# Kernel tuning notes

Measured on AMD Instinct MI355X. Metric: run time of the kernel, lower is better.

## Reference

```python
import jax, jax.numpy as jnp
import numpy as np

N_NODES = 100000
N_EDGES = 1600000


def setup_inputs() -> dict:
    key = jax.random.key(0)
    ks = jax.random.split(key, 6)
    x = jax.random.normal(ks[0], (N_NODES, 128), dtype=jnp.float32)
    edge_src = jax.random.randint(ks[1], (N_EDGES,), 0, N_NODES, dtype=jnp.int64)
    edge_dst = jax.random.randint(ks[2], (N_EDGES,), 0, N_NODES, dtype=jnp.int64)
    # GCNConv weights (bias=False); glorot-like scaling
    W1 = jax.random.normal(ks[3], (128, 64), dtype=jnp.float32) * (1.0 / np.sqrt(128))
    W2 = jax.random.normal(ks[4], (64, 64), dtype=jnp.float32) * (1.0 / np.sqrt(64))
    W3 = jax.random.normal(ks[5], (64, 40), dtype=jnp.float32) * (1.0 / np.sqrt(64))
    return {"x": x, "edge_src": edge_src, "edge_dst": edge_dst,
            "W1": W1, "W2": W2, "W3": W3}


def reference(x, edge_src, edge_dst, W1, W2, W3):
    # SGC forward (eval mode: dropout is identity).
    # Each GCNConv(normalize=False, bias=False): out = A @ (h @ W)
    n = x.shape[0]

    def conv(h, W):
        hw = h @ W                      # [N, d_out] dense transform
        msgs = hw[edge_src]             # [E, d_out] gather over edges
        return jax.ops.segment_sum(msgs, edge_dst, num_segments=n)  # scatter-add

    h = conv(x, W1)
    h = conv(h, W2)
    h = conv(h, W3)
    return jax.nn.log_softmax(h, axis=-1)
```

## Files before the change

kernel.cpp:

```cpp
#include <hip/hip_runtime.h>
#include <hip/hip_fp16.h>
#include <math.h>


#define BW    128
#define NBMAX 1024
#define BCAP  3072
#define D     40
#define RS    64

typedef unsigned short u16;
typedef unsigned int   u32;

__global__ void k_w12(const float* __restrict__ W1, const float* __restrict__ W2,
                      float* __restrict__ W12, int* __restrict__ gcnt) {
    int idx = blockIdx.x * blockDim.x + threadIdx.x;
    if (blockIdx.x == 0) {
        for (int i = threadIdx.x; i < NBMAX; i += blockDim.x) gcnt[i] = 0;
    }
    if (idx >= 128 * 64) return;
    int r = idx >> 6, c = idx & 63;
    float acc = 0.f;
#pragma unroll
    for (int k = 0; k < 64; ++k) acc += W1[r * 64 + k] * W2[k * 64 + c];
    W12[idx] = acc;
}

__global__ void k_wc(const float* __restrict__ W12, const float* __restrict__ W3,
                     float* __restrict__ Wc) {
    int idx = blockIdx.x * blockDim.x + threadIdx.x;
    if (idx >= 128 * 40) return;
    int r = idx / 40, c = idx - r * 40;
    float acc = 0.f;
#pragma unroll
    for (int k = 0; k < 64; ++k) acc += W12[r * 64 + k] * W3[k * 40 + c];
    Wc[idx] = acc;
}

__global__ void k_gemm(const float4* __restrict__ x4, const float4* __restrict__ Wc4,
                       u16* __restrict__ yout, int n_nodes) {
    __shared__ float4 wc[128 * 10];
    for (int i = threadIdx.x; i < 1280; i += blockDim.x) wc[i] = Wc4[i];
    __syncthreads();
    int tid = blockIdx.x * blockDim.x + threadIdx.x;
    int node = tid / 5, j0 = tid - node * 5;
    if (node >= n_nodes) return;
    float4 a0 = {0.f, 0.f, 0.f, 0.f}, a1 = {0.f, 0.f, 0.f, 0.f};
    const float4* xr = x4 + (size_t)node * 32;
#pragma unroll
    for (int k4 = 0; k4 < 32; ++k4) {
        float4 v = xr[k4];
#pragma unroll
        for (int kk = 0; kk < 4; ++kk) {
            float c = (kk == 0) ? v.x : (kk == 1) ? v.y : (kk == 2) ? v.z : v.w;
            float4 w0 = wc[(k4 * 4 + kk) * 10 + j0 * 2];
            float4 w1 = wc[(k4 * 4 + kk) * 10 + j0 * 2 + 1];
            a0.x += c * w0.x; a0.y += c * w0.y; a0.z += c * w0.z; a0.w += c * w0.w;
            a1.x += c * w1.x; a1.y += c * w1.y; a1.z += c * w1.z; a1.w += c * w1.w;
        }
    }
    __half2 h0 = __floats2half2_rn(a0.x, a0.y);
    __half2 h1 = __floats2half2_rn(a0.z, a0.w);
    __half2 h2 = __floats2half2_rn(a1.x, a1.y);
    __half2 h3 = __floats2half2_rn(a1.z, a1.w);
    uint4 st;
    st.x = *(u32*)&h0; st.y = *(u32*)&h1; st.z = *(u32*)&h2; st.w = *(u32*)&h3;
    *(uint4*)(yout + (size_t)node * RS + j0 * 8) = st;
}

#define PCHUNK 2048
__global__ void k_part(const int* __restrict__ src, const int* __restrict__ dst,
                       int* __restrict__ gcnt, int* __restrict__ part,
                       int E, int nb) {
    __shared__ int h[NBMAX];
    __shared__ int base[NBMAX];
    int t = threadIdx.x;
    int e0 = blockIdx.x * PCHUNK;
    int e1 = min(e0 + PCHUNK, E);
    for (int i = t; i < nb; i += 256) h[i] = 0;
    __syncthreads();
    for (int e = e0 + t; e < e1; e += 256)
        atomicAdd(&h[dst[e] >> 7], 1);
    __syncthreads();
    for (int i = t; i < nb; i += 256) {
        int c = h[i];
        base[i] = c ? atomicAdd(&gcnt[i], c) : 0;
    }
    __syncthreads();
    for (int i = t; i < nb; i += 256) h[i] = 0;
    __syncthreads();
    for (int e = e0 + t; e < e1; e += 256) {
        int d = dst[e];
        int b = d >> 7;
        int p = base[b] + atomicAdd(&h[b], 1);
        if (p < BCAP) part[(size_t)b * BCAP + p] = (src[e] << 7) | (d & 127);
    }
}

__global__ void k_csr(const int* __restrict__ part, const int* __restrict__ gcnt,
                      int* __restrict__ begv, int* __restrict__ endv,
                      int* __restrict__ ssort, int N) {
    __shared__ int cnt[BW];
    __shared__ int pos[BW];
    __shared__ int cur[BW];
    __shared__ int wsum[2];
    int b = blockIdx.x, t = threadIdx.x;
    int m = min(gcnt[b], BCAP);
    const int* bp = part + (size_t)b * BCAP;
    if (t < BW) cnt[t] = 0;
    __syncthreads();
    for (int k = t; k < m; k += 256)
        atomicAdd(&cnt[bp[k] & 127], 1);
    __syncthreads();
    int v = 0, inc = 0;
    if (t < BW) {
        v = cnt[t];
        inc = v;
#pragma unroll
        for (int off = 1; off < 64; off <<= 1) {
            int u = __shfl_up(inc, off, 64);
            if ((t & 63) >= off) inc += u;
        }
        if ((t & 63) == 63) wsum[t >> 6] = inc;
    }
    __syncthreads();
    int node0 = b * BW;
    if (t < BW) {
        int local = ((t >= 64) ? wsum[0] : 0) + inc - v;
        pos[t] = local;
        cur[t] = 0;
        if (node0 + t < N) {
            begv[node0 + t] = b * BCAP + local;
            endv[node0 + t] = b * BCAP + local + v;
        }
    }
    __syncthreads();
    for (int k = t; k < m; k += 256) {
        int p = bp[k];
        int r = p & 127;
        int loc = atomicAdd(&cur[r], 1);
        ssort[(size_t)b * BCAP + pos[r] + loc] = p >> 7;
    }
}

template <int FINAL>
__global__ void k_agg(const u16* __restrict__ yin, void* __restrict__ youtv,
                      const int* __restrict__ begv, const int* __restrict__ endv,
                      const int* __restrict__ srcs, int n_nodes) {
    int wid = (blockIdx.x * blockDim.x + threadIdx.x) >> 6;
    int lane = threadIdx.x & 63;
    if (wid >= n_nodes) return;
    int beg = begv[wid];
    int deg = endv[wid] - beg;
    int g = lane / 10;
    int sub = lane - g * 10;
    bool act = (g < 6);
    const char* base = (const char*)yin + sub * 8;
    int sv = (lane < deg) ? srcs[beg + lane] : 0;
    __half2 c0 = __floats2half2_rn(0.f, 0.f);
    __half2 c1 = __floats2half2_rn(0.f, 0.f);
    int dlim = min(deg, 64);
    for (int k = 0; k < dlim; k += 24) {
#pragma unroll
        for (int j = 0; j < 4; ++j) {
            int e = k + g + 6 * j;
            int es = (e < dlim) ? e : 0;
            int s = __shfl(sv, es, 64);
            if (act && e < dlim) {
                uint2 w = *(const uint2*)(base + (size_t)((u32)s * 128u));
                c0 = __hadd2(c0, *(__half2*)&w.x);
                c1 = __hadd2(c1, *(__half2*)&w.y);
            }
        }
    }
    for (int k = 64 + g; k < deg; k += 6) {
        if (act) {
            uint2 w = *(const uint2*)(base + (size_t)((u32)srcs[beg + k] * 128u));
            c0 = __hadd2(c0, *(__half2*)&w.x);
            c1 = __hadd2(c1, *(__half2*)&w.y);
        }
    }
    float2 f0 = __half22float2(c0);
    float2 f1 = __half22float2(c1);
    float a0 = f0.x, a1 = f0.y, a2 = f1.x, a3 = f1.y;
    float b0 = a0 + __shfl(a0, lane + 30, 64);
    float b1 = a1 + __shfl(a1, lane + 30, 64);
    float b2 = a2 + __shfl(a2, lane + 30, 64);
    float b3 = a3 + __shfl(a3, lane + 30, 64);
    float s0 = b0 + __shfl(b0, lane + 10, 64) + __shfl(b0, lane + 20, 64);
    float s1 = b1 + __shfl(b1, lane + 10, 64) + __shfl(b1, lane + 20, 64);
    float s2 = b2 + __shfl(b2, lane + 10, 64) + __shfl(b2, lane + 20, 64);
    float s3 = b3 + __shfl(b3, lane + 10, 64) + __shfl(b3, lane + 20, 64);
    if (FINAL) {
        float m = fmaxf(fmaxf(s0, s1), fmaxf(s2, s3));
        float mv = (lane < 10) ? m : -INFINITY;
#pragma unroll
        for (int off = 8; off; off >>= 1) mv = fmaxf(mv, __shfl_xor(mv, off, 16));
        float ev = 0.f;
        if (lane < 10)
            ev = __expf(s0 - mv) + __expf(s1 - mv) + __expf(s2 - mv) + __expf(s3 - mv);
#pragma unroll
        for (int off = 8; off; off >>= 1) ev += __shfl_xor(ev, off, 16);
        float ls = __logf(ev);
        if (lane < 10) {
            float4 o = {s0 - mv - ls, s1 - mv - ls, s2 - mv - ls, s3 - mv - ls};
            ((float4*)((float*)youtv + (size_t)wid * D))[sub] = o;
        }
    } else {
        if (lane < 10) {
            __half2 h0 = __floats2half2_rn(s0, s1);
            __half2 h1 = __floats2half2_rn(s2, s3);
            uint2 st = {*(u32*)&h0, *(u32*)&h1};
            *(uint2*)((u16*)youtv + (size_t)wid * RS + sub * 4) = st;
        }
    }
}

extern "C" void kernel_launch(void* const* d_in, const int* in_sizes, int n_in,
                              void* d_out, int out_size, void* d_ws, size_t ws_size,
                              hipStream_t stream) {
    const float* x   = (const float*)d_in[0];
    const int* esrc  = (const int*)d_in[1];
    const int* edst  = (const int*)d_in[2];
    const float* W1  = (const float*)d_in[3];
    const float* W2  = (const float*)d_in[4];
    const float* W3  = (const float*)d_in[5];
    int N = in_sizes[0] / 128;
    int E = in_sizes[1];
    float* out = (float*)d_out;

    int nb = (N + BW - 1) / BW;

    char* ws = (char*)d_ws;
    auto alloc = [&](size_t bytes) {
        char* p = ws;
        ws += (bytes + 255) & ~(size_t)255;
        return p;
    };
    u16* bufA   = (u16*)alloc((size_t)N * RS * sizeof(u16));
    u16* bufB   = (u16*)alloc((size_t)N * RS * sizeof(u16));
    int* part   = (int*)bufB;
    int* ssort  = (int*)alloc((size_t)nb * BCAP * sizeof(int));
    int* begv   = (int*)alloc((size_t)N * sizeof(int));
    int* endv   = (int*)alloc((size_t)N * sizeof(int));
    float* W12  = (float*)alloc(128 * 64 * sizeof(float));
    float* Wc   = (float*)alloc(128 * 40 * sizeof(float));
    int* gcnt   = (int*)alloc(NBMAX * sizeof(int));

    k_w12<<<(128 * 64 + 255) / 256, 256, 0, stream>>>(W1, W2, W12, gcnt);
    k_wc<<<(128 * 40 + 255) / 256, 256, 0, stream>>>(W12, W3, Wc);
    k_gemm<<<(N * 5 + 255) / 256, 256, 0, stream>>>((const float4*)x, (const float4*)Wc,
                                                    bufA, N);

    k_part<<<(E + PCHUNK - 1) / PCHUNK, 256, 0, stream>>>(esrc, edst, gcnt, part, E, nb);
    k_csr<<<nb, 256, 0, stream>>>(part, gcnt, begv, endv, ssort, N);

    int agg_grid = (N * 64 + 255) / 256;
    k_agg<0><<<agg_grid, 256, 0, stream>>>(bufA, bufB, begv, endv, ssort, N);
    k_agg<0><<<agg_grid, 256, 0, stream>>>(bufB, bufA, begv, endv, ssort, N);
    k_agg<1><<<agg_grid, 256, 0, stream>>>(bufA, out, begv, endv, ssort, N);
}
```

Baseline: 202.6 us.

## Pack 12 nodes per wavefront in aggregation and unroll partition scatter

The aggregation kernel now gives each group of 5 lanes one node, so a wavefront handles 12 nodes. Each lane loads 16 bytes (8 halves) per neighbor, and there is no cross-group reduction. Before, one wavefront served one node and only 60 of its 64 lanes were active, which wasted lanes on low-degree nodes and needed shuffle reductions. The partition kernel's scatter loop is also unrolled 4x to batch its independent loads and atomics. The cost is divergence: a wavefront's loop runs until its highest-degree node among the 12 finishes.

```diff
diff --git a/kernel.cpp b/kernel.cpp
--- a/kernel.cpp
+++ b/kernel.cpp
@@ -8,9 +8,16 @@
 #define BCAP  3072
 #define D     40
 #define RS    64
+#define NPW   12
 
 typedef unsigned short u16;
 typedef unsigned int   u32;
+
+static __device__ inline u32 hadd2u(u32 a, u32 b) {
+    __half2 ha = *(__half2*)&a, hb = *(__half2*)&b;
+    __half2 r = __hadd2(ha, hb);
+    return *(u32*)&r;
+}
 
 __global__ void k_w12(const float* __restrict__ W1, const float* __restrict__ W2,
                       float* __restrict__ W12, int* __restrict__ gcnt) {
@@ -89,11 +96,21 @@
     __syncthreads();
     for (int i = t; i < nb; i += 256) h[i] = 0;
     __syncthreads();
-    for (int e = e0 + t; e < e1; e += 256) {
-        int d = dst[e];
-        int b = d >> 7;
-        int p = base[b] + atomicAdd(&h[b], 1);
-        if (p < BCAP) part[(size_t)b * BCAP + p] = (src[e] << 7) | (d & 127);
+    for (int e = e0 + t; e < e1; e += 1024) {
+        bool v1 = (e + 256) < e1, v2 = (e + 512) < e1, v3 = (e + 768) < e1;
+        int d0 = dst[e], s0 = src[e];
+        int d1 = v1 ? dst[e + 256] : 0, s1 = v1 ? src[e + 256] : 0;
+        int d2 = v2 ? dst[e + 512] : 0, s2 = v2 ? src[e + 512] : 0;
+        int d3 = v3 ? dst[e + 768] : 0, s3 = v3 ? src[e + 768] : 0;
+        int b0 = d0 >> 7, b1 = d1 >> 7, b2 = d2 >> 7, b3 = d3 >> 7;
+        int p0 = base[b0] + atomicAdd(&h[b0], 1);
+        int p1 = v1 ? (base[b1] + atomicAdd(&h[b1], 1)) : BCAP;
+        int p2 = v2 ? (base[b2] + atomicAdd(&h[b2], 1)) : BCAP;
+        int p3 = v3 ? (base[b3] + atomicAdd(&h[b3], 1)) : BCAP;
+        if (p0 < BCAP) part[(size_t)b0 * BCAP + p0] = (s0 << 7) | (d0 & 127);
+        if (p1 < BCAP) part[(size_t)b1 * BCAP + p1] = (s1 << 7) | (d1 & 127);
+        if (p2 < BCAP) part[(size_t)b2 * BCAP + p2] = (s2 << 7) | (d2 & 127);
+        if (p3 < BCAP) part[(size_t)b3 * BCAP + p3] = (s3 << 7) | (d3 & 127);
     }
 }
 
@@ -149,69 +166,60 @@
                       const int* __restrict__ srcs, int n_nodes) {
     int wid = (blockIdx.x * blockDim.x + threadIdx.x) >> 6;
     int lane = threadIdx.x & 63;
-    if (wid >= n_nodes) return;
-    int beg = begv[wid];
-    int deg = endv[wid] - beg;
-    int g = lane / 10;
-    int sub = lane - g * 10;
-    bool act = (g < 6);
-    const char* base = (const char*)yin + sub * 8;
-    int sv = (lane < deg) ? srcs[beg + lane] : 0;
-    __half2 c0 = __floats2half2_rn(0.f, 0.f);
-    __half2 c1 = __floats2half2_rn(0.f, 0.f);
-    int dlim = min(deg, 64);
-    for (int k = 0; k < dlim; k += 24) {
-#pragma unroll
-        for (int j = 0; j < 4; ++j) {
-            int e = k + g + 6 * j;
-            int es = (e < dlim) ? e : 0;
-            int s = __shfl(sv, es, 64);
-            if (act && e < dlim) {
-                uint2 w = *(const uint2*)(base + (size_t)((u32)s * 128u));
-                c0 = __hadd2(c0, *(__half2*)&w.x);
-                c1 = __hadd2(c1, *(__half2*)&w.y);
+    int g = lane / 5;
+    int sub = lane - g * 5;
+    int node = wid * NPW + g;
+    bool nv = (g < NPW) && (node < n_nodes);
+    int ncl = nv ? node : 0;
+    int beg = begv[ncl];
+    int deg = nv ? (endv[ncl] - beg) : 0;
+    u32 suboff = (u32)sub * 16u;
+    u32 c0 = 0, c1 = 0, c2 = 0, c3 = 0;
+    for (int k = 0; __any(k < deg); k += 5) {
+        int sv = (k + sub < deg) ? srcs[beg + k + sub] : 0;
+#pragma unroll
+        for (int j = 0; j < 5; ++j) {
+            int s = __shfl(sv, g * 5 + j, 64);
+            if (k + j < deg) {
+                uint4 w = *(const uint4*)((const char*)yin +
+                              (size_t)(((u32)s << 7) + suboff));
+                c0 = hadd2u(c0, w.x); c1 = hadd2u(c1, w.y);
+                c2 = hadd2u(c2, w.z); c3 = hadd2u(c3, w.w);
             }
         }
     }
-    for (int k = 64 + g; k < deg; k += 6) {
-        if (act) {
-            uint2 w = *(const uint2*)(base + (size_t)((u32)srcs[beg + k] * 128u));
-            c0 = __hadd2(c0, *(__half2*)&w.x);
-            c1 = __hadd2(c1, *(__half2*)&w.y);
-        }
-    }
-    float2 f0 = __half22float2(c0);
-    float2 f1 = __half22float2(c1);
-    float a0 = f0.x, a1 = f0.y, a2 = f1.x, a3 = f1.y;
-    float b0 = a0 + __shfl(a0, lane + 30, 64);
-    float b1 = a1 + __shfl(a1, lane + 30, 64);
-    float b2 = a2 + __shfl(a2, lane + 30, 64);
-    float b3 = a3 + __shfl(a3, lane + 30, 64);
-    float s0 = b0 + __shfl(b0, lane + 10, 64) + __shfl(b0, lane + 20, 64);
-    float s1 = b1 + __shfl(b1, lane + 10, 64) + __shfl(b1, lane + 20, 64);
-    float s2 = b2 + __shfl(b2, lane + 10, 64) + __shfl(b2, lane + 20, 64);
-    float s3 = b3 + __shfl(b3, lane + 10, 64) + __shfl(b3, lane + 20, 64);
     if (FINAL) {
-        float m = fmaxf(fmaxf(s0, s1), fmaxf(s2, s3));
-        float mv = (lane < 10) ? m : -INFINITY;
-#pragma unroll
-        for (int off = 8; off; off >>= 1) mv = fmaxf(mv, __shfl_xor(mv, off, 16));
-        float ev = 0.f;
-        if (lane < 10)
-            ev = __expf(s0 - mv) + __expf(s1 - mv) + __expf(s2 - mv) + __expf(s3 - mv);
-#pragma unroll
-        for (int off = 8; off; off >>= 1) ev += __shfl_xor(ev, off, 16);
-        float ls = __logf(ev);
-        if (lane < 10) {
-            float4 o = {s0 - mv - ls, s1 - mv - ls, s2 - mv - ls, s3 - mv - ls};
-            ((float4*)((float*)youtv + (size_t)wid * D))[sub] = o;
+        float2 f0 = __half22float2(*(__half2*)&c0);
+        float2 f1 = __half22float2(*(__half2*)&c1);
+        float2 f2 = __half22float2(*(__half2*)&c2);
+        float2 f3 = __half22float2(*(__half2*)&c3);
+        int s1 = sub + 1; s1 = (s1 >= 5) ? s1 - 5 : s1;
+        int s2 = sub + 2; s2 = (s2 >= 5) ? s2 - 5 : s2;
+        int s4 = sub + 4; s4 = (s4 >= 5) ? s4 - 5 : s4;
+        int r1 = g * 5 + s1, r2 = g * 5 + s2, r4 = g * 5 + s4;
+        float m0 = fmaxf(fmaxf(fmaxf(f0.x, f0.y), fmaxf(f1.x, f1.y)),
+                         fmaxf(fmaxf(f2.x, f2.y), fmaxf(f3.x, f3.y)));
+        float m = fmaxf(m0, __shfl(m0, r1, 64));
+        m = fmaxf(m, __shfl(m, r2, 64));
+        m = fmaxf(m, __shfl(m0, r4, 64));
+        float e0 = __expf(f0.x - m) + __expf(f0.y - m) + __expf(f1.x - m) +
+                   __expf(f1.y - m) + __expf(f2.x - m) + __expf(f2.y - m) +
+                   __expf(f3.x - m) + __expf(f3.y - m);
+        float sm = e0 + __shfl(e0, r1, 64);
+        sm = sm + __shfl(sm, r2, 64);
+        sm = sm + __shfl(e0, r4, 64);
+        float ls = __logf(sm) + m;
+        if (nv) {
+            float4 o1 = {f0.x - ls, f0.y - ls, f1.x - ls, f1.y - ls};
+            float4 o2 = {f2.x - ls, f2.y - ls, f3.x - ls, f3.y - ls};
+            float* op = (float*)youtv + (size_t)node * D + sub * 8;
+            *(float4*)op = o1;
+            *(float4*)(op + 4) = o2;
         }
     } else {
-        if (lane < 10) {
-            __half2 h0 = __floats2half2_rn(s0, s1);
-            __half2 h1 = __floats2half2_rn(s2, s3);
-            uint2 st = {*(u32*)&h0, *(u32*)&h1};
-            *(uint2*)((u16*)youtv + (size_t)wid * RS + sub * 4) = st;
+        if (nv) {
+            uint4 st = {c0, c1, c2, c3};
+            *(uint4*)((u16*)youtv + (size_t)node * RS + sub * 8) = st;
         }
     }
 }
@@ -255,7 +263,8 @@
     k_part<<<(E + PCHUNK - 1) / PCHUNK, 256, 0, stream>>>(esrc, edst, gcnt, part, E, nb);
     k_csr<<<nb, 256, 0, stream>>>(part, gcnt, begv, endv, ssort, N);
 
-    int agg_grid = (N * 64 + 255) / 256;
+    int nwaves = (N + NPW - 1) / NPW;
+    int agg_grid = (nwaves + 3) / 4;
     k_agg<0><<<agg_grid, 256, 0, stream>>>(bufA, bufB, begv, endv, ssort, N);
     k_agg<0><<<agg_grid, 256, 0, stream>>>(bufB, bufA, begv, endv, ssort, N);
     k_agg<1><<<agg_grid, 256, 0, stream>>>(bufA, out, begv, endv, ssort, N);
```

Result: faster. 195.7 us (-3.4%).
